# Optimization experiments

Hardware: AMD Instinct MI355X
Metric: run time of the kernel (lower is better)

Reference implementation:

```python
import jax, jax.numpy as jnp
import numpy as np

D = 768
N_TASKS = 4


def setup_inputs() -> dict:
    key = jax.random.key(0)
    k1, k2, k3, k4, k5 = jax.random.split(key, 5)
    b, s, t = 8, 1024, 1024
    source_features = jax.random.normal(k1, (b, s, D), dtype=jnp.float32)
    target_features = jax.random.normal(k2, (b, t, D), dtype=jnp.float32)
    # learned params: nn.Linear(768,1) + Sigmoid, nn.Embedding(4,768), alpha
    W_cost = jax.random.normal(k3, (D, 1), dtype=jnp.float32) / np.sqrt(D)
    b_cost = jnp.zeros((1,), dtype=jnp.float32)
    task_emb = jax.random.normal(k4, (N_TASKS, D), dtype=jnp.float32)
    alpha = jnp.float32(0.05)
    return {
        "source_features": source_features,
        "target_features": target_features,
        "W_cost": W_cost,
        "b_cost": b_cost,
        "task_emb": task_emb,
        "alpha": alpha,
        "task_id": 2,
    }


def reference(source_features, target_features, W_cost, b_cost, task_emb, alpha, task_id):
    # metric='cosine': elementwise cos of the raw dot-product matrix (as in source)
    dots = jnp.einsum("bsd,btd->bst", source_features, target_features)
    cost = (1.0 - jnp.cos(dots)) / 2.0  # [b,s,t]

    # use_kernel_cost=True: gaussian kernel with h = 1 * std (unbiased, over last two dims)
    std = jnp.std(cost, axis=(-1, -2), keepdims=True, ddof=1)
    cost = jnp.exp(-((cost / std) ** 2) / 2.0)

    # train_cost_matrix=True: conditional MLP on (src + tgt + task_fea), Linear(768,1)+Sigmoid.
    # Linear is applied before the nonlinearity, so decompose to avoid the [b,s,t,768] tensor.
    s_proj = jnp.einsum("bsd,d->bs", source_features, W_cost[:, 0])  # [b,s]
    t_proj = jnp.einsum("btd,d->bt", target_features, W_cost[:, 0])  # [b,t]
    task_proj = jnp.dot(task_emb[task_id], W_cost[:, 0])  # scalar
    cond = jax.nn.sigmoid(
        s_proj[:, :, None] + t_proj[:, None, :] + task_proj + b_cost[0]
    )  # [b,s,t]

    cost = alpha * (cost + cond)
    return cost
```

## Files before the change

### kernel.cpp

```cpp
#include <hip/hip_runtime.h>
#include <hip/hip_bf16.h>
#include <math.h>

#define BATCHES 8
#define SEQ 1024
#define DDIM 768
#define NPANEL 16
#define NK64 12
#define CHUNK_B 8192
#define NK32 24
#define QMAX 6.35f

typedef unsigned short u16;
typedef __attribute__((ext_vector_type(8))) short bf16x8;
typedef __attribute__((ext_vector_type(8))) unsigned short u16x8;
typedef __attribute__((ext_vector_type(4))) float f32x4;
typedef __attribute__((ext_vector_type(4))) int i32x4;

static __device__ __forceinline__ u16 f2bf(float x) {
    union { float f; unsigned u; } v; v.f = x;
    unsigned r = v.u + 0x7FFFu + ((v.u >> 16) & 1u);
    return (u16)(r >> 16);
}
static __device__ __forceinline__ float bf2f(u16 h) {
    union { float f; unsigned u; } v; v.u = ((unsigned)h) << 16; return v.f;
}

__global__ __launch_bounds__(256) void prep_i8(
    const float* __restrict__ S, const float* __restrict__ T,
    const float* __restrict__ W, const float* __restrict__ bcost,
    const float* __restrict__ temb, const int* __restrict__ task_id,
    unsigned char* __restrict__ Sg, unsigned char* __restrict__ Tg,
    float* __restrict__ sproj, float* __restrict__ tproj,
    float* __restrict__ cterm)
{
    int t = threadIdx.x;
    int g = blockIdx.x * 256 + t;
    int r  = g & 15;
    int kg = (g >> 4) & 3;
    int m  = (g >> 6) & 3;
    int x  = g >> 8;
    int ks = x % NK64;
    int y  = x / NK64;
    int p  = y & 15;
    int b  = (y >> 4) & 7;
    int tensor = y >> 7;

    int row_loc = p * 64 + m * 16 + r;
    int row_glb = b * SEQ + row_loc;
    int col = ks * 64 + kg * 16;

    const float* src = (tensor ? T : S) + (size_t)row_glb * DDIM + col;
    float4 f0 = *(const float4*)(src);
    float4 f1 = *(const float4*)(src + 4);
    float4 f2 = *(const float4*)(src + 8);
    float4 f3 = *(const float4*)(src + 12);
    float4 w0 = *(const float4*)(W + col);
    float4 w1 = *(const float4*)(W + col + 4);
    float4 w2 = *(const float4*)(W + col + 8);
    float4 w3 = *(const float4*)(W + col + 12);

    float xv[16] = {f0.x,f0.y,f0.z,f0.w, f1.x,f1.y,f1.z,f1.w,
                    f2.x,f2.y,f2.z,f2.w, f3.x,f3.y,f3.z,f3.w};
    float wv[16] = {w0.x,w0.y,w0.z,w0.w, w1.x,w1.y,w1.z,w1.w,
                    w2.x,w2.y,w2.z,w2.w, w3.x,w3.y,w3.z,w3.w};

    float pd = 0.f;
    #pragma unroll
    for (int e = 0; e < 16; ++e) pd = fmaf(xv[e], wv[e], pd);
    pd += __shfl_down(pd, 32);
    pd += __shfl_down(pd, 16);
    if ((t & 63) < 16)
        atomicAdd((tensor ? tproj : sproj) + row_glb, pd);

    const float s     = QMAX / 127.0f;
    const float inv_s = 127.0f / QMAX;
    const float inv_s2 = 252.0f / s;
    unsigned q1w[4] = {0,0,0,0}, q2w[4] = {0,0,0,0};
    #pragma unroll
    for (int e = 0; e < 16; ++e) {
        float v = xv[e];
        float q1f = rintf(v * inv_s);
        q1f = fminf(fmaxf(q1f, -127.f), 127.f);
        float rr = fmaf(-q1f, s, v);
        float q2f = rintf(rr * inv_s2);
        q2f = fminf(fmaxf(q2f, -126.f), 126.f);
        unsigned b1 = (unsigned)(unsigned char)(char)(int)q1f;
        unsigned b2 = (unsigned)(unsigned char)(char)(int)q2f;
        q1w[e >> 2] |= b1 << ((e & 3) * 8);
        q2w[e >> 2] |= b2 << ((e & 3) * 8);
    }
    unsigned char* dst = (tensor ? Tg : Sg)
        + (size_t)((b * NPANEL + p) * NK64 + ks) * CHUNK_B
        + (m * 1024 + kg * 256 + r * 16);
    *(uint4*)dst          = (uint4){q1w[0], q1w[1], q1w[2], q1w[3]};
    *(uint4*)(dst + 4096) = (uint4){q2w[0], q2w[1], q2w[2], q2w[3]};

    if (blockIdx.x == 0 && t < 64) {
        int tid = *task_id;
        float sacc = 0.f;
        #pragma unroll
        for (int d = t; d < DDIM; d += 64) sacc = fmaf(temb[tid * DDIM + d], W[d], sacc);
        #pragma unroll
        for (int o = 32; o; o >>= 1) sacc += __shfl_down(sacc, o);
        if (t == 0) *cterm = sacc + bcost[0];
    }
}

__global__ __launch_bounds__(256) void proj_kernel(
    const float* __restrict__ S, const float* __restrict__ T,
    const float* __restrict__ W, const float* __restrict__ bcost,
    const float* __restrict__ temb, const int* __restrict__ task_id,
    float* __restrict__ sproj, float* __restrict__ tproj,
    float* __restrict__ cterm)
{
    int gw   = (blockIdx.x * blockDim.x + threadIdx.x) >> 6;
    int lane = threadIdx.x & 63;

    if (gw < 2 * BATCHES * SEQ) {
        const float* rowp = (gw < BATCHES * SEQ)
            ? S + (size_t)gw * DDIM
            : T + (size_t)(gw - BATCHES * SEQ) * DDIM;
        float s = 0.f;
        #pragma unroll
        for (int d = lane; d < DDIM; d += 64) s = fmaf(rowp[d], W[d], s);
        #pragma unroll
        for (int o = 32; o; o >>= 1) s += __shfl_down(s, o);
        if (lane == 0) {
            if (gw < BATCHES * SEQ) sproj[gw] = s;
            else                    tproj[gw - BATCHES * SEQ] = s;
        }
    }
    if (blockIdx.x == gridDim.x - 1 && (threadIdx.x >> 6) == 0) {
        int tid = *task_id;
        float s = 0.f;
        #pragma unroll
        for (int d = lane; d < DDIM; d += 64) s = fmaf(temb[tid * DDIM + d], W[d], s);
        #pragma unroll
        for (int o = 32; o; o >>= 1) s += __shfl_down(s, o);
        if (lane == 0) *cterm = s + bcost[0];
    }
}

__global__ __launch_bounds__(256, 4) void gemm_i8(
    const unsigned char* __restrict__ Sg, const unsigned char* __restrict__ Tg,
    _Float16* __restrict__ c0buf, double* __restrict__ batch_sums)
{
    __shared__ double red[8];

    const int t    = threadIdx.x;
    const int lane = t & 63;
    const int w    = t >> 6;

    const int b   = blockIdx.x & 7;
    const int q   = blockIdx.x >> 3;
    const int bx  = q & 15;
    const int byh = ((q >> 4) << 2) + w;
    const int p   = byh >> 1;
    const int h   = byh & 1;

    i32x4 acc_hh[2][4], acc_x[2][4];
    #pragma unroll
    for (int m = 0; m < 2; ++m)
        #pragma unroll
        for (int n = 0; n < 4; ++n) {
            acc_hh[m][n] = (i32x4){0,0,0,0};
            acc_x[m][n]  = (i32x4){0,0,0,0};
        }

    const unsigned char* Achunk = Sg + (size_t)((b * NPANEL + p) * NK64) * CHUNK_B
                                + (h * 2) * 1024 + lane * 16;
    const unsigned char* Bchunk = Tg + (size_t)((b * NPANEL + bx) * NK64) * CHUNK_B
                                + lane * 16;

    #pragma unroll 1
    for (int ks = 0; ks < NK64; ++ks) {
        const unsigned char* Ak = Achunk + (size_t)ks * CHUNK_B;
        const unsigned char* Bk = Bchunk + (size_t)ks * CHUNK_B;
        i32x4 a1[2], a2[2], b1[4], b2[4];
        #pragma unroll
        for (int m = 0; m < 2; ++m) {
            a1[m] = *(const i32x4*)(Ak + m * 1024);
            a2[m] = *(const i32x4*)(Ak + 4096 + m * 1024);
        }
        #pragma unroll
        for (int n = 0; n < 4; ++n) {
            b1[n] = *(const i32x4*)(Bk + n * 1024);
            b2[n] = *(const i32x4*)(Bk + 4096 + n * 1024);
        }
        #pragma unroll
        for (int m = 0; m < 2; ++m)
            #pragma unroll
            for (int n = 0; n < 4; ++n) {
                acc_hh[m][n] = __builtin_amdgcn_mfma_i32_16x16x64_i8(a1[m], b1[n], acc_hh[m][n], 0, 0, 0);
                acc_x[m][n]  = __builtin_amdgcn_mfma_i32_16x16x64_i8(a1[m], b2[n], acc_x[m][n], 0, 0, 0);
                acc_x[m][n]  = __builtin_amdgcn_mfma_i32_16x16x64_i8(a2[m], b1[n], acc_x[m][n], 0, 0, 0);
            }
        __builtin_amdgcn_s_barrier();
    }

    const float S2  = (QMAX / 127.0f) * (QMAX / 127.0f);
    const float S2F = S2 / 252.0f;
    float lsum = 0.f, lsq = 0.f;
    _Float16* cb = c0buf + (size_t)b * SEQ * SEQ;
    const int rbase = byh * 32;
    const int cbase = bx * 64;
    const int cr = lane >> 4;
    const int cc = lane & 15;
    #pragma unroll
    for (int m = 0; m < 2; ++m) {
        #pragma unroll
        for (int n = 0; n < 4; ++n) {
            int col = cbase + n * 16 + cc;
            #pragma unroll
            for (int j = 0; j < 4; ++j) {
                int row = rbase + m * 16 + cr * 4 + j;
                float d  = S2 * (float)acc_hh[m][n][j] + S2F * (float)acc_x[m][n][j];
                float c0 = 0.5f - 0.5f * __cosf(d);
                cb[(size_t)row * SEQ + col] = (_Float16)c0;
                lsum += c0;
                lsq  = fmaf(c0, c0, lsq);
            }
        }
    }

    double s = (double)lsum, q2 = (double)lsq;
    #pragma unroll
    for (int o = 32; o; o >>= 1) { s += __shfl_down(s, o); q2 += __shfl_down(q2, o); }
    if (lane == 0) { red[w] = s; red[4 + w] = q2; }
    __syncthreads();
    if (t == 0) {
        s  = red[0] + red[1] + red[2] + red[3];
        q2 = red[4] + red[5] + red[6] + red[7];
        atomicAdd(&batch_sums[b * 2 + 0], s);
        atomicAdd(&batch_sums[b * 2 + 1], q2);
    }
}

__global__ __launch_bounds__(256) void gemm_fused_bf16(
    const float* __restrict__ S, const float* __restrict__ T,
    float* __restrict__ out, double* __restrict__ batch_sums)
{
    __shared__ __align__(16) u16 lds[16384];
    __shared__ double red[8];

    const int t    = threadIdx.x;
    const int lane = t & 63;
    const int w    = t >> 6;
    const int wr   = w >> 1, wc = w & 1;

    int wg = (blockIdx.x & 7) * 64 + (blockIdx.x >> 3);
    const int b  = wg >> 6;
    const int by = (wg >> 3) & 7;
    const int bx = wg & 7;

    f32x4 acc[4][4];
    #pragma unroll
    for (int m = 0; m < 4; ++m)
        #pragma unroll
        for (int n = 0; n < 4; ++n) acc[m][n] = (f32x4){0.f, 0.f, 0.f, 0.f};

    const float* Sb = S + (size_t)b * SEQ * DDIM;
    const float* Tb = T + (size_t)b * SEQ * DDIM;
    const float* pa[2]; const float* pb[2];
    float4 ra[2][2], rb[2][2];
    #pragma unroll
    for (int i = 0; i < 2; ++i) {
        int g = t + i * 256;
        int m = g >> 6, kg = (g >> 4) & 3, r = g & 15;
        pa[i] = Sb + (size_t)(by * 128 + m * 16 + r) * DDIM + kg * 8;
        pb[i] = Tb + (size_t)(bx * 128 + m * 16 + r) * DDIM + kg * 8;
    }

    auto LOADREGS = [&](int ks) {
        #pragma unroll
        for (int i = 0; i < 2; ++i) {
            ra[i][0] = *(const float4*)(pa[i] + ks * 32);
            ra[i][1] = *(const float4*)(pa[i] + ks * 32 + 4);
            rb[i][0] = *(const float4*)(pb[i] + ks * 32);
            rb[i][1] = *(const float4*)(pb[i] + ks * 32 + 4);
        }
    };
    auto STAGE_FUSED = [&]() {
        #pragma unroll
        for (int i = 0; i < 2; ++i) {
            int g = t + i * 256;
            float xa[8] = {ra[i][0].x, ra[i][0].y, ra[i][0].z, ra[i][0].w,
                           ra[i][1].x, ra[i][1].y, ra[i][1].z, ra[i][1].w};
            float xb[8] = {rb[i][0].x, rb[i][0].y, rb[i][0].z, rb[i][0].w,
                           rb[i][1].x, rb[i][1].y, rb[i][1].z, rb[i][1].w};
            u16x8 ah, al, bh, bl;
            #pragma unroll
            for (int e = 0; e < 8; ++e) {
                u16 h = f2bf(xa[e]); ah[e] = h; al[e] = f2bf(xa[e] - bf2f(h));
                u16 g2 = f2bf(xb[e]); bh[e] = g2; bl[e] = f2bf(xb[e] - bf2f(g2));
            }
            *(u16x8*)&lds[(size_t)g * 8]         = ah;
            *(u16x8*)&lds[4096 + (size_t)g * 8]  = al;
            *(u16x8*)&lds[8192 + (size_t)g * 8]  = bh;
            *(u16x8*)&lds[12288 + (size_t)g * 8] = bl;
        }
    };
    auto COMPUTE = [&]() {
        const u16* L = &lds[0];
        bf16x8 ah[4], al[4], bh[4], bl[4];
        #pragma unroll
        for (int m = 0; m < 4; ++m) {
            int sm = wr * 4 + m;
            ah[m] = *(const bf16x8*)(L + sm * 512 + lane * 8);
            al[m] = *(const bf16x8*)(L + 4096 + sm * 512 + lane * 8);
        }
        #pragma unroll
        for (int n = 0; n < 4; ++n) {
            int sn = wc * 4 + n;
            bh[n] = *(const bf16x8*)(L + 8192 + sn * 512 + lane * 8);
            bl[n] = *(const bf16x8*)(L + 12288 + sn * 512 + lane * 8);
        }
        #pragma unroll
        for (int m = 0; m < 4; ++m)
            #pragma unroll
            for (int n = 0; n < 4; ++n) {
                acc[m][n] = __builtin_amdgcn_mfma_f32_16x16x32_bf16(ah[m], bh[n], acc[m][n], 0, 0, 0);
                acc[m][n] = __builtin_amdgcn_mfma_f32_16x16x32_bf16(ah[m], bl[n], acc[m][n], 0, 0, 0);
                acc[m][n] = __builtin_amdgcn_mfma_f32_16x16x32_bf16(al[m], bh[n], acc[m][n], 0, 0, 0);
            }
    };

    LOADREGS(0);
    for (int ks = 0; ks < NK32; ++ks) {
        STAGE_FUSED();
        __syncthreads();
        if (ks + 1 < NK32) LOADREGS(ks + 1);
        COMPUTE();
        __syncthreads();
    }

    float lsum = 0.f, lsq = 0.f;
    float* outb = out + (size_t)b * SEQ * SEQ;
    const int rbase = by * 128 + wr * 64;
    const int cbase = bx * 128 + wc * 64;
    const int cr = lane >> 4;
    const int cc = lane & 15;
    #pragma unroll
    for (int m = 0; m < 4; ++m) {
        #pragma unroll
        for (int n = 0; n < 4; ++n) {
            int col = cbase + n * 16 + cc;
            #pragma unroll
            for (int j = 0; j < 4; ++j) {
                int row = rbase + m * 16 + cr * 4 + j;
                float d  = acc[m][n][j];
                float c0 = 0.5f - 0.5f * __cosf(d);
                outb[(size_t)row * SEQ + col] = c0;
                lsum += c0;
                lsq  = fmaf(c0, c0, lsq);
            }
        }
    }

    double s = (double)lsum, q = (double)lsq;
    #pragma unroll
    for (int o = 32; o; o >>= 1) { s += __shfl_down(s, o); q += __shfl_down(q, o); }
    if (lane == 0) { red[w] = s; red[4 + w] = q; }
    __syncthreads();
    if (t == 0) {
        s = red[0] + red[1] + red[2] + red[3];
        q = red[4] + red[5] + red[6] + red[7];
        atomicAdd(&batch_sums[b * 2 + 0], s);
        atomicAdd(&batch_sums[b * 2 + 1], q);
    }
}

__global__ __launch_bounds__(256) void finalize_half(
    float* __restrict__ out, const _Float16* __restrict__ c0buf,
    const double* __restrict__ batch_sums,
    const float* __restrict__ sproj, const float* __restrict__ tproj,
    const float* __restrict__ cterm_p, const float* __restrict__ alpha_p)
{
    const double n = (double)SEQ * (double)SEQ;
    size_t idx8 = (size_t)blockIdx.x * blockDim.x + threadIdx.x;
    size_t base = idx8 * 8;
    int batch = (int)(base >> 20);
    int rem   = (int)(base & ((SEQ * SEQ) - 1));
    int srow  = rem >> 10;
    int tcol  = rem & (SEQ - 1);

    double sum = batch_sums[batch * 2 + 0];
    double sq  = batch_sums[batch * 2 + 1];
    double var = (sq - sum * sum / n) / (n - 1.0);
    float inv_std = (float)(1.0 / sqrt(var));

    float alpha = *alpha_p;
    float ct    = *cterm_p;
    float sp    = sproj[batch * SEQ + srow] + ct;
    float4 tp0  = *(const float4*)&tproj[batch * SEQ + tcol];
    float4 tp1  = *(const float4*)&tproj[batch * SEQ + tcol + 4];

    _Float16 h[8];
    *(uint4*)h = *(const uint4*)(c0buf + base);
    float tps[8] = {tp0.x, tp0.y, tp0.z, tp0.w, tp1.x, tp1.y, tp1.z, tp1.w};
    float r[8];
    #pragma unroll
    for (int e = 0; e < 8; ++e) {
        float x = (float)h[e] * inv_std;
        float g = __expf(-0.5f * x * x);
        float z = sp + tps[e];
        float cd = 1.f / (1.f + __expf(-z));
        r[e] = alpha * (g + cd);
    }
    *(float4*)&out[base]     = (float4){r[0], r[1], r[2], r[3]};
    *(float4*)&out[base + 4] = (float4){r[4], r[5], r[6], r[7]};
}

__global__ __launch_bounds__(256) void finalize_f32(
    float* __restrict__ out, const double* __restrict__ batch_sums,
    const float* __restrict__ sproj, const float* __restrict__ tproj,
    const float* __restrict__ cterm_p, const float* __restrict__ alpha_p)
{
    const double n = (double)SEQ * (double)SEQ;
    size_t idx4 = (size_t)blockIdx.x * blockDim.x + threadIdx.x;
    size_t base = idx4 * 4;
    int batch = (int)(base >> 20);
    int rem   = (int)(base & ((SEQ * SEQ) - 1));
    int srow  = rem >> 10;
    int tcol  = rem & (SEQ - 1);

    double sum = batch_sums[batch * 2 + 0];
    double sq  = batch_sums[batch * 2 + 1];
    double var = (sq - sum * sum / n) / (n - 1.0);
    float inv_std = (float)(1.0 / sqrt(var));

    float alpha = *alpha_p;
    float ct    = *cterm_p;
    float sp    = sproj[batch * SEQ + srow];
    float4 tp   = *(const float4*)&tproj[batch * SEQ + tcol];
    float4 c    = *(float4*)&out[base];

    float4 r;
    { float x = c.x * inv_std; float g = __expf(-0.5f * x * x);
      float z = sp + tp.x + ct; float cd = 1.f / (1.f + __expf(-z)); r.x = alpha * (g + cd); }
    { float x = c.y * inv_std; float g = __expf(-0.5f * x * x);
      float z = sp + tp.y + ct; float cd = 1.f / (1.f + __expf(-z)); r.y = alpha * (g + cd); }
    { float x = c.z * inv_std; float g = __expf(-0.5f * x * x);
      float z = sp + tp.z + ct; float cd = 1.f / (1.f + __expf(-z)); r.z = alpha * (g + cd); }
    { float x = c.w * inv_std; float g = __expf(-0.5f * x * x);
      float z = sp + tp.w + ct; float cd = 1.f / (1.f + __expf(-z)); r.w = alpha * (g + cd); }
    *(float4*)&out[base] = r;
}

extern "C" void kernel_launch(void* const* d_in, const int* in_sizes, int n_in,
                              void* d_out, int out_size, void* d_ws, size_t ws_size,
                              hipStream_t stream) {
    const float* S      = (const float*)d_in[0];
    const float* T      = (const float*)d_in[1];
    const float* W      = (const float*)d_in[2];
    const float* bcost  = (const float*)d_in[3];
    const float* temb   = (const float*)d_in[4];
    const float* alpha  = (const float*)d_in[5];
    const int*   taskid = (const int*)d_in[6];
    float* out = (float*)d_out;

    double* batch_sums = (double*)d_ws;
    float*  sproj = (float*)((char*)d_ws + 128);
    float*  tproj = sproj + BATCHES * SEQ;
    float*  cterm = tproj + BATCHES * SEQ;

    const size_t ZERO_BYTES = 128 + sizeof(float) * (2 * BATCHES * SEQ + 1);
    const size_t SMALL = (size_t)1 << 20;
    const size_t CONV_B = (size_t)BATCHES * NPANEL * NK64 * CHUNK_B;
    const size_t C0_B   = (size_t)BATCHES * SEQ * SEQ * 2;
    const size_t NEEDED = SMALL + 2 * CONV_B + C0_B;
    unsigned char* Sg = (unsigned char*)d_ws + SMALL;
    unsigned char* Tg = Sg + CONV_B;
    _Float16* c0buf = (_Float16*)(Tg + CONV_B);

    hipMemsetAsync(d_ws, 0, ZERO_BYTES, stream);

    if (ws_size >= NEEDED) {
        int nblk = (2 * BATCHES * NPANEL * NK64 * 256) / 256;
        prep_i8<<<nblk, 256, 0, stream>>>(S, T, W, bcost, temb, taskid,
                                          Sg, Tg, sproj, tproj, cterm);
        gemm_i8<<<1024, 256, 0, stream>>>(Sg, Tg, c0buf, batch_sums);
        int nfin = (BATCHES * SEQ * SEQ) / (256 * 8);
        finalize_half<<<nfin, 256, 0, stream>>>(out, c0buf, batch_sums,
                                                sproj, tproj, cterm, alpha);
    } else {
        proj_kernel<<<4097, 256, 0, stream>>>(S, T, W, bcost, temb, taskid,
                                              sproj, tproj, cterm);
        gemm_fused_bf16<<<512, 256, 0, stream>>>(S, T, out, batch_sums);
        int nfin = (BATCHES * SEQ * SEQ) / (256 * 4);
        finalize_f32<<<nfin, 256, 0, stream>>>(out, batch_sums, sproj, tproj,
                                               cterm, alpha);
    }
}
```

Baseline: 65.72 us.

## Double-buffer B tiles in LDS via direct global-to-LDS loads in int8 GEMM

The shared B tile, which every wave previously loaded from global memory on its own, is now staged cooperatively into LDS with global_load_lds. Two ping-pong buffers let the next k-slice load while the current one feeds the MFMAs. This targets redundant global traffic for B across the four waves and the load latency that sat in front of compute. In exchange it adds 16 KB of LDS per block, which may limit occupancy at 4 blocks/CU, plus full vmcnt(0) waits and barriers every half-iteration that can serialize the pipeline.

```diff
diff --git a/kernel.cpp b/kernel.cpp
--- a/kernel.cpp
+++ b/kernel.cpp
@@ -24,6 +24,12 @@
 }
 static __device__ __forceinline__ float bf2f(u16 h) {
     union { float f; unsigned u; } v; v.u = ((unsigned)h) << 16; return v.f;
+}
+
+__device__ __forceinline__ void glds16(const void* g, void* l) {
+    __builtin_amdgcn_global_load_lds(
+        (const __attribute__((address_space(1))) void*)g,
+        (__attribute__((address_space(3))) void*)l, 16, 0, 0);
 }
 
 __global__ __launch_bounds__(256) void prep_i8(
@@ -146,6 +152,8 @@
     const unsigned char* __restrict__ Sg, const unsigned char* __restrict__ Tg,
     _Float16* __restrict__ c0buf, double* __restrict__ batch_sums)
 {
+    __shared__ __align__(16) unsigned char bufA[8192];
+    __shared__ __align__(16) unsigned char bufB[8192];
     __shared__ double red[8];
 
     const int t    = threadIdx.x;
@@ -171,12 +179,15 @@
     const unsigned char* Achunk = Sg + (size_t)((b * NPANEL + p) * NK64) * CHUNK_B
                                 + (h * 2) * 1024 + lane * 16;
     const unsigned char* Bchunk = Tg + (size_t)((b * NPANEL + bx) * NK64) * CHUNK_B
-                                + lane * 16;
-
-    #pragma unroll 1
-    for (int ks = 0; ks < NK64; ++ks) {
+                                + w * 2048 + lane * 16;
+
+    auto STAGE_B = [&](int ks, unsigned char* buf) {
+        const unsigned char* src = Bchunk + (size_t)ks * CHUNK_B;
+        glds16(src,        buf + w * 2048);
+        glds16(src + 1024, buf + w * 2048 + 1024);
+    };
+    auto COMPUTE = [&](int ks, const unsigned char* buf) {
         const unsigned char* Ak = Achunk + (size_t)ks * CHUNK_B;
-        const unsigned char* Bk = Bchunk + (size_t)ks * CHUNK_B;
         i32x4 a1[2], a2[2], b1[4], b2[4];
         #pragma unroll
         for (int m = 0; m < 2; ++m) {
@@ -185,8 +196,8 @@
         }
         #pragma unroll
         for (int n = 0; n < 4; ++n) {
-            b1[n] = *(const i32x4*)(Bk + n * 1024);
-            b2[n] = *(const i32x4*)(Bk + 4096 + n * 1024);
+            b1[n] = *(const i32x4*)(buf + n * 1024 + lane * 16);
+            b2[n] = *(const i32x4*)(buf + 4096 + n * 1024 + lane * 16);
         }
         #pragma unroll
         for (int m = 0; m < 2; ++m)
@@ -196,6 +207,20 @@
                 acc_x[m][n]  = __builtin_amdgcn_mfma_i32_16x16x64_i8(a1[m], b2[n], acc_x[m][n], 0, 0, 0);
                 acc_x[m][n]  = __builtin_amdgcn_mfma_i32_16x16x64_i8(a2[m], b1[n], acc_x[m][n], 0, 0, 0);
             }
+    };
+
+    STAGE_B(0, bufA);
+    asm volatile("s_waitcnt vmcnt(0)" ::: "memory");
+    __builtin_amdgcn_s_barrier();
+    #pragma unroll 1
+    for (int it = 0; it < NK64; it += 2) {
+        STAGE_B(it + 1, bufB);
+        COMPUTE(it, bufA);
+        asm volatile("s_waitcnt vmcnt(0) lgkmcnt(0)" ::: "memory");
+        __builtin_amdgcn_s_barrier();
+        if (it + 2 < NK64) STAGE_B(it + 2, bufA);
+        COMPUTE(it + 1, bufB);
+        asm volatile("s_waitcnt vmcnt(0) lgkmcnt(0)" ::: "memory");
         __builtin_amdgcn_s_barrier();
     }
 
```

Result: no change. 66.90 us (+1.8%).
